# Performance work log

Measured on AMD Instinct MI355X. Metric: run time of the kernel, lower is better.

## Reference

```python
import jax, jax.numpy as jnp
import numpy as np

B, S, HID, NH, DH = 2, 1024, 4096, 32, 128
ACT_BITS, W_BITS = 8, 4
NEG_INF = float(np.finfo(np.float32).min)


def _qdq(x, bits):
    """Symmetric fake-quant over the last axis (per-token / per-out-channel), with STE."""
    qmax = 2.0 ** (bits - 1) - 1
    s = jnp.maximum(jnp.max(jnp.abs(x), axis=-1, keepdims=True) / qmax, 1e-8)
    q = jnp.clip(jnp.round(x / s), -qmax - 1, qmax) * s
    return x + jax.lax.stop_gradient(q - x)


def _rope_tables(seq_len, dim):
    inv_freq = 1.0 / (10000.0 ** (np.arange(0, dim, 2, dtype=np.float32) / dim))
    t = np.arange(seq_len, dtype=np.float32)
    freqs = np.outer(t, inv_freq)              # [S, DH/2]
    emb = np.concatenate([freqs, freqs], -1)   # [S, DH]
    return jnp.asarray(np.cos(emb)), jnp.asarray(np.sin(emb))


def _rotate_half(x):
    h = x.shape[-1] // 2
    return jnp.concatenate([-x[..., h:], x[..., :h]], axis=-1)


def _norm(x):
    return jnp.linalg.norm(x, axis=-1, keepdims=True)


def setup_inputs() -> dict:
    key = jax.random.key(0)
    ks = jax.random.split(key, 5)
    causal = jnp.where(jnp.tril(jnp.ones((S, S), dtype=bool)), 0.0, NEG_INF).astype(jnp.float32)
    return {
        "hidden_states": jax.random.normal(ks[0], (B, S, HID), jnp.float32),
        "wq": jax.random.normal(ks[1], (HID, HID), jnp.float32) * 0.02,
        "wk": jax.random.normal(ks[2], (HID, HID), jnp.float32) * 0.02,
        "wv": jax.random.normal(ks[3], (HID, HID), jnp.float32) * 0.02,
        "wo": jax.random.normal(ks[4], (HID, HID), jnp.float32) * 0.02,
        "attention_mask": jnp.broadcast_to(causal[None, None], (B, 1, S, S)),
    }


def reference(hidden_states, wq, wk, wv, wo, attention_mask):
    cos, sin = _rope_tables(S, DH)
    cos, sin = cos[None, None], sin[None, None]          # [1,1,S,DH]
    x = _qdq(hidden_states, ACT_BITS)                    # act fake-quant (per token)

    def proj(w):
        return jnp.einsum('bsh,dh->bsd', x, _qdq(w, W_BITS)).reshape(B, S, NH, DH).transpose(0, 2, 1, 3)

    q, k, v = proj(wq), proj(wk), proj(wv)               # [B,H,S,D]
    q = q * cos + _rotate_half(q) * sin
    k = k * cos + _rotate_half(k) * sin

    # qkt_matmul: quant Q and K, rescale scores by quantization norm ratios a1, a2
    x1len = _norm(q)
    qq = _qdq(q, ACT_BITS)
    a1 = _norm(qq) / x1len                               # [B,H,S,1]
    x2len = _norm(k)
    kq = _qdq(k, ACT_BITS)
    a2 = jnp.swapaxes(_norm(kq) / x2len, 2, 3)           # [B,H,1,S]

    attn = jnp.einsum('bhqd,bhkd->bhqk', qq, kq) / np.float32(np.sqrt(DH))
    attn = attn / a1 / a2
    attn = attn + attention_mask
    attn = jnp.maximum(attn, NEG_INF)
    p = jax.nn.softmax(attn.astype(jnp.float32), axis=-1)

    # pv_matmul: quant P and V, rescale output by V's norm ratio
    pq = _qdq(p, ACT_BITS)
    x2len_v = _norm(v)
    vq = _qdq(v, ACT_BITS)
    a2v = _norm(vq) / x2len_v                            # [B,H,S,1]

    out = jnp.einsum('bhqk,bhkd->bhqd', pq, vq) / a2v    # [B,H,S,D]
    out = out.transpose(0, 2, 1, 3).reshape(B, S, HID)
    out = jnp.einsum('bsh,dh->bsd', _qdq(out, ACT_BITS), _qdq(wo, W_BITS))
    return out
```

## Files before the change

kernel.cpp:

```cpp
#include <hip/hip_runtime.h>
#include <hip/hip_bf16.h>
#include <math.h>
#include <stdint.h>

#define NEG_INF_F (-3.4028234663852886e38f)

typedef __bf16 bf16_t;
typedef __bf16 bf16x8 __attribute__((ext_vector_type(8)));
typedef float f32x4 __attribute__((ext_vector_type(4)));
typedef float f32x16 __attribute__((ext_vector_type(16)));
typedef int i32x4 __attribute__((ext_vector_type(4)));
typedef int i32x16 __attribute__((ext_vector_type(16)));
typedef int8_t c8x4 __attribute__((ext_vector_type(4)));

static constexpr int Bb = 2, Ss = 1024, Hid = 4096, Nh = 32, Dh = 128;
static constexpr int Mr = Bb * Ss;
static constexpr int Bh = Bb * Nh;

__device__ __forceinline__ void gload_lds16(const void* g, void* l) {
  __builtin_amdgcn_global_load_lds((const __attribute__((address_space(1))) void*)g,
                                   (__attribute__((address_space(3))) void*)l, 16, 0, 0);
}

__device__ __forceinline__ float wred_max(float v) {
#pragma unroll
  for (int off = 32; off > 0; off >>= 1) v = fmaxf(v, __shfl_xor(v, off));
  return v;
}

__device__ __forceinline__ unsigned pkbf(float a, float b) {
  unsigned short ua = __builtin_bit_cast(unsigned short, (bf16_t)a);
  unsigned short ub = __builtin_bit_cast(unsigned short, (bf16_t)b);
  return (unsigned)ua | ((unsigned)ub << 16);
}

__global__ void rope_table_kernel(float* __restrict__ ctab, float* __restrict__ stab) {
  int i = blockIdx.x * 256 + threadIdx.x;
  int srow = i >> 6, d = i & 63;
  float invf = (float)pow(10000.0, -((double)(2 * d) / (double)Dh));
  float ang = (float)srow * invf;
  ctab[i] = (float)cos((double)ang);
  stab[i] = (float)sin((double)ang);
}

__device__ __forceinline__ void quant_row_body(
    const float* __restrict__ x, int8_t* __restrict__ o, float* __restrict__ scale,
    int row, int ncols, float qmax, float clo, float chi)
{
  const int tid = threadIdx.x;
  const float4* x4 = (const float4*)x;
  const int n4 = ncols >> 2;
  float m = 0.f;
  for (int i = tid; i < n4; i += 256) {
    float4 v = x4[i];
    m = fmaxf(m, fmaxf(fmaxf(fabsf(v.x), fabsf(v.y)), fmaxf(fabsf(v.z), fabsf(v.w))));
  }
  m = wred_max(m);
  __shared__ float red[4];
  if ((tid & 63) == 0) red[tid >> 6] = m;
  __syncthreads();
  m = fmaxf(fmaxf(red[0], red[1]), fmaxf(red[2], red[3]));
  const float s = fmaxf(m / qmax, 1e-8f);
  if (tid == 0) scale[row] = s;
  c8x4* o4 = (c8x4*)o;
  for (int i = tid; i < n4; i += 256) {
    float4 v = x4[i];
    c8x4 r;
    r[0] = (int8_t)(int)fminf(fmaxf(rintf(v.x / s), clo), chi);
    r[1] = (int8_t)(int)fminf(fmaxf(rintf(v.y / s), clo), chi);
    r[2] = (int8_t)(int)fminf(fmaxf(rintf(v.z / s), clo), chi);
    r[3] = (int8_t)(int)fminf(fmaxf(rintf(v.w / s), clo), chi);
    o4[i] = r;
  }
}

__global__ __launch_bounds__(256) void quant_rows_kernel(
    const float* __restrict__ in, int8_t* __restrict__ outq,
    float* __restrict__ scale, int ncols, float qmax, float clo, float chi)
{
  const int row = blockIdx.x;
  quant_row_body(in + (size_t)row * ncols, outq + (size_t)row * ncols, scale,
                 row, ncols, qmax, clo, chi);
}

__global__ __launch_bounds__(256) void quant_w3_kernel(
    const float* __restrict__ w0, const float* __restrict__ w1, const float* __restrict__ w2,
    int8_t* __restrict__ o0, int8_t* __restrict__ o1, int8_t* __restrict__ o2,
    float* __restrict__ s0, float* __restrict__ s1, float* __restrict__ s2)
{
  const int sel = blockIdx.x >> 12, row = blockIdx.x & 4095;
  const float* in = sel == 0 ? w0 : (sel == 1 ? w1 : w2);
  int8_t* o = sel == 0 ? o0 : (sel == 1 ? o1 : o2);
  float* sc = sel == 0 ? s0 : (sel == 1 ? s1 : s2);
  quant_row_body(in + (size_t)row * Hid, o + (size_t)row * Hid, sc, row, Hid,
                 7.f, -8.f, 7.f);
}

#define GEMM_PHASE(Abuf, Bbuf)                                                        \
  {                                                                                   \
    i32x4 af[4], bw[4];                                                               \
    _Pragma("unroll")                                                                 \
    for (int f = 0; f < 4; ++f) {                                                     \
      af[f] = *(const i32x4*)&(Abuf)[(wm * 64 + f * 16 + l15) * 64 + ck];             \
      bw[f] = *(const i32x4*)&(Bbuf)[(f * 32 + wn * 16 + l15) * 64 + ck];             \
    }                                                                                 \
    _Pragma("unroll")                                                                 \
    for (int fm = 0; fm < 4; ++fm)                                                    \
      _Pragma("unroll")                                                               \
      for (int fn = 0; fn < 4; ++fn)                                                  \
        acc[fm][fn] = __builtin_amdgcn_mfma_i32_16x16x64_i8(af[fm], bw[fn],           \
                                                            acc[fm][fn], 0, 0, 0);   \
  }

#define GEMM_STAGE(koff, Abuf, Bbuf)                                                  \
  gload_lds16(gA + (koff), (Abuf) + wid * 1024);                                      \
  gload_lds16(gA + (koff) + rstep, (Abuf) + 4096 + wid * 1024);                       \
  gload_lds16(gB + (koff), (Bbuf) + wid * 1024);                                      \
  gload_lds16(gB + (koff) + rstep, (Bbuf) + 4096 + wid * 1024);

#define GEMM_CORE_DBUF(SMEM)                                                          \
  int8_t* A0 = (int8_t*)(SMEM);                                                       \
  int8_t* A1 = (int8_t*)(SMEM) + 8192;                                                \
  int8_t* B0 = (int8_t*)(SMEM) + 16384;                                               \
  int8_t* B1 = (int8_t*)(SMEM) + 24576;                                               \
  const int srowL = tid >> 2;                                                         \
  const int schunk = ((tid & 3) ^ ((tid >> 3) & 3)) * 16;                             \
  const int8_t* gA = A + (size_t)(bm + srowL) * K + schunk;                           \
  const int8_t* gB = W + (size_t)(bn + srowL) * K + schunk;                           \
  const size_t rstep = (size_t)64 * K;                                                \
  const int ck = (kg4 ^ ((l15 >> 1) & 3)) * 16;                                       \
  i32x4 acc[4][4] = {};                                                               \
  GEMM_STAGE(0, A0, B0)                                                               \
  __syncthreads();                                                                    \
  for (int k0 = 0; k0 < K; k0 += 128) {                                               \
    if (k0 + 64 < K) { GEMM_STAGE(k0 + 64, A1, B1) }                                  \
    GEMM_PHASE(A0, B0)                                                                \
    __syncthreads();                                                                  \
    if (k0 + 128 < K) { GEMM_STAGE(k0 + 128, A0, B0) }                                \
    GEMM_PHASE(A1, B1)                                                                \
    __syncthreads();                                                                  \
  }

__global__ __launch_bounds__(256) void qkv_gemm_kernel(
    const int8_t* __restrict__ A, const float* __restrict__ sA,
    const int8_t* __restrict__ wqz, const int8_t* __restrict__ wkz, const int8_t* __restrict__ wvz,
    const float* __restrict__ swq, const float* __restrict__ swk, const float* __restrict__ swv,
    int8_t* __restrict__ qqb, float* __restrict__ Fq,
    int8_t* __restrict__ kqb, float* __restrict__ Fk,
    bf16_t* __restrict__ vdq, float* __restrict__ a2vp,
    const float* __restrict__ ctab, const float* __restrict__ stab)
{
  __shared__ __align__(16) char smem[34816 + 3072];
  float (*s_red)[128][3] = (float (*)[128][3])(smem + 34816);

  const int tid = threadIdx.x, lane = tid & 63, wid = tid >> 6;
  const int id = blockIdx.x;
  const int xcd = id & 7, within = id >> 3;
  const int nIdx = xcd * 12 + (within >> 4);
  const int mIdx = within & 15;
  const int wsel = nIdx >> 5, head = nIdx & 31;
  const int bm = mIdx * 128, bn = head * 128;
  const int8_t* W = wsel == 0 ? wqz : (wsel == 1 ? wkz : wvz);
  const float* sW = wsel == 0 ? swq : (wsel == 1 ? swk : swv);
  constexpr int K = Hid;

  const int wm = wid >> 1, wn = wid & 1;
  const int l15 = lane & 15, kg4 = lane >> 4;

  GEMM_CORE_DBUF(smem)

  float sav[4][4], swv_[4];
#pragma unroll
  for (int fm = 0; fm < 4; ++fm)
#pragma unroll
    for (int j = 0; j < 4; ++j) sav[fm][j] = sA[bm + wm * 64 + fm * 16 + kg4 * 4 + j];
#pragma unroll
  for (int fn = 0; fn < 4; ++fn) swv_[fn] = sW[bn + fn * 32 + wn * 16 + l15];

  float val[4][4][4];
#pragma unroll
  for (int fm = 0; fm < 4; ++fm)
#pragma unroll
    for (int fn = 0; fn < 4; ++fn)
#pragma unroll
      for (int j = 0; j < 4; ++j)
        val[fm][fn][j] = (float)acc[fm][fn][j] * sav[fm][j] * swv_[fn];

  const int b = bm >> 10;
  const int bh = b * Nh + head;
  float r_[4][4][4];
  if (wsel != 2) {
    const int dmA = wn * 16 + l15, dmB = 32 + wn * 16 + l15;
#pragma unroll
    for (int fm = 0; fm < 4; ++fm)
#pragma unroll
      for (int j = 0; j < 4; ++j) {
        const int srow = (bm + wm * 64 + fm * 16 + kg4 * 4 + j) & (Ss - 1);
        const float cA = ctab[srow * 64 + dmA], cB = ctab[srow * 64 + dmB];
        const float sA_ = stab[srow * 64 + dmA], sB_ = stab[srow * 64 + dmB];
        r_[fm][0][j] = __fsub_rn(__fmul_rn(val[fm][0][j], cA), __fmul_rn(val[fm][2][j], sA_));
        r_[fm][1][j] = __fsub_rn(__fmul_rn(val[fm][1][j], cB), __fmul_rn(val[fm][3][j], sB_));
        r_[fm][2][j] = __fadd_rn(__fmul_rn(val[fm][2][j], cA), __fmul_rn(val[fm][0][j], sA_));
        r_[fm][3][j] = __fadd_rn(__fmul_rn(val[fm][3][j], cB), __fmul_rn(val[fm][1][j], sB_));
      }
  } else {
#pragma unroll
    for (int fm = 0; fm < 4; ++fm)
#pragma unroll
      for (int fn = 0; fn < 4; ++fn)
#pragma unroll
        for (int j = 0; j < 4; ++j) r_[fm][fn][j] = val[fm][fn][j];
  }
  float ma_[4][4], n2_[4][4];
#pragma unroll
  for (int fm = 0; fm < 4; ++fm)
#pragma unroll
    for (int j = 0; j < 4; ++j) {
      float ma = 0.f, n2 = 0.f;
#pragma unroll
      for (int fn = 0; fn < 4; ++fn) {
        const float x = r_[fm][fn][j];
        ma = fmaxf(ma, fabsf(x));
        n2 += x * x;
      }
#pragma unroll
      for (int off = 1; off < 16; off <<= 1) {
        ma = fmaxf(ma, __shfl_xor(ma, off));
        n2 += __shfl_xor(n2, off);
      }
      ma_[fm][j] = ma;
      n2_[fm][j] = n2;
    }
  if (l15 == 0) {
#pragma unroll
    for (int fm = 0; fm < 4; ++fm)
#pragma unroll
      for (int j = 0; j < 4; ++j) {
        const int rl = wm * 64 + fm * 16 + kg4 * 4 + j;
        s_red[wn][rl][0] = ma_[fm][j];
        s_red[wn][rl][1] = n2_[fm][j];
      }
  }
  __syncthreads();
  float qc[4][4][4], svl[4][4], n2c[4][4], nq2_[4][4];
#pragma unroll
  for (int fm = 0; fm < 4; ++fm)
#pragma unroll
    for (int j = 0; j < 4; ++j) {
      const int rl = wm * 64 + fm * 16 + kg4 * 4 + j;
      const float ma = fmaxf(ma_[fm][j], s_red[wn ^ 1][rl][0]);
      const float n2 = n2_[fm][j] + s_red[wn ^ 1][rl][1];
      const float s = fmaxf(ma / 127.0f, 1e-8f);
      float nq2 = 0.f;
#pragma unroll
      for (int fn = 0; fn < 4; ++fn) {
        const float q = fminf(fmaxf(rintf(r_[fm][fn][j] / s), -128.f), 127.f);
        qc[fm][fn][j] = q;
        nq2 += q * q;
      }
#pragma unroll
      for (int off = 1; off < 16; off <<= 1) nq2 += __shfl_xor(nq2, off);
      svl[fm][j] = s;
      n2c[fm][j] = n2;
      nq2_[fm][j] = nq2;
    }
  __syncthreads();
  if (l15 == 0) {
#pragma unroll
    for (int fm = 0; fm < 4; ++fm)
#pragma unroll
      for (int j = 0; j < 4; ++j)
        s_red[wn][wm * 64 + fm * 16 + kg4 * 4 + j][2] = nq2_[fm][j];
  }
  __syncthreads();

  if (wsel != 2) {
    int8_t* outq = (wsel == 0) ? qqb : kqb;
    float* Ff = (wsel == 0) ? Fq : Fk;
#pragma unroll
    for (int fm = 0; fm < 4; ++fm)
#pragma unroll
      for (int j = 0; j < 4; ++j) {
        const int rl = wm * 64 + fm * 16 + kg4 * 4 + j;
        const int stok = (bm + rl) & (Ss - 1);
        const size_t rowBase = ((size_t)bh * Ss + stok) * Dh;
#pragma unroll
        for (int fn = 0; fn < 4; ++fn)
          outq[rowBase + fn * 32 + wn * 16 + l15] = (int8_t)(int)qc[fm][fn][j];
        if (wn == 0 && l15 == 0) {
          const float nq2 = nq2_[fm][j] + s_red[1][rl][2];
          Ff[(size_t)bh * Ss + stok] = sqrtf(n2c[fm][j] / nq2) * 0.2973017787506803f;
        }
      }
  } else {
    bf16_t* svt = (bf16_t*)smem;
#pragma unroll
    for (int fm = 0; fm < 4; ++fm)
#pragma unroll
      for (int j = 0; j < 4; ++j) {
        const int t = wm * 64 + fm * 16 + kg4 * 4 + j;
#pragma unroll
        for (int fn = 0; fn < 4; ++fn) {
          const int d = fn * 32 + wn * 16 + l15;
          svt[d * 136 + t] = (bf16_t)(qc[fm][fn][j] * svl[fm][j]);
        }
        if (wn == 0 && l15 == 0) {
          const float nq2 = nq2_[fm][j] + s_red[1][t][2];
          a2vp[(size_t)bh * Ss + ((bm + t) & (Ss - 1))] =
              svl[fm][j] * sqrtf(nq2) / sqrtf(n2c[fm][j]);
        }
      }
    __syncthreads();
    const int d = tid >> 1, toff = (tid & 1) * 64;
    const int s0 = bm & (Ss - 1);
    const bf16_t* src = svt + d * 136 + toff;
    bf16_t* dst = vdq + ((size_t)bh * Dh + d) * Ss + s0 + toff;
#pragma unroll
    for (int k = 0; k < 8; ++k) {
      bf16x8 tv;
#pragma unroll
      for (int e = 0; e < 8; ++e) tv[e] = src[k * 8 + e];
      *(bf16x8*)(dst + k * 8) = tv;
    }
  }
}

__global__ __launch_bounds__(256) void gemm0_kernel(
    const int8_t* __restrict__ A, const float* __restrict__ sA,
    const int8_t* __restrict__ W, const float* __restrict__ sW,
    float* __restrict__ out, int M, int N, int K)
{
  __shared__ __align__(16) char smem[32768];
  const int tid = threadIdx.x, lane = tid & 63, wid = tid >> 6;
  const int id = blockIdx.x;
  const int xcd = id & 7, within = id >> 3;
  const int nIdx = xcd * 4 + (within >> 4);
  const int mIdx = within & 15;
  const int bm = mIdx * 128, bn = nIdx * 128;
  const int wm = wid >> 1, wn = wid & 1;
  const int l15 = lane & 15, kg4 = lane >> 4;

  GEMM_CORE_DBUF(smem)

#pragma unroll
  for (int fm = 0; fm < 4; ++fm) {
#pragma unroll
    for (int j = 0; j < 4; ++j) {
      const int row = bm + wm * 64 + fm * 16 + kg4 * 4 + j;
      const float sa = sA[row];
#pragma unroll
      for (int fn = 0; fn < 4; ++fn) {
        const int col = bn + fn * 32 + wn * 16 + l15;
        out[(size_t)row * N + col] = (float)acc[fm][fn][j] * sa * sW[col];
      }
    }
  }
}

#define KR(r) (((r) & 3) + 8 * ((r) >> 2) + 4 * hi)
__global__ __launch_bounds__(64, 2) void attn_kernel(
    const int8_t* __restrict__ qq, const int8_t* __restrict__ kq,
    const bf16_t* __restrict__ vdqt,
    const float* __restrict__ Fq, const float* __restrict__ Fk,
    const float* __restrict__ A2v, float* __restrict__ oattn)
{
  const int bh = blockIdx.x, b = bh >> 5, h = bh & 31;
  const int lane = threadIdx.x & 63;
  const int l31 = lane & 31, hi = lane >> 5;
  const int u = 31 - (int)blockIdx.y;
  const int q0 = u * 32;
  const int nt = u + 1;
  const size_t bhS = (size_t)bh * Ss;

  const int8_t* qrow = qq + (bhS + q0 + l31) * Dh + hi * 16;
  i32x4 qf[4];
#pragma unroll
  for (int c = 0; c < 4; ++c) qf[c] = *(const i32x4*)(qrow + c * 32);
  const float fq = Fq[bhS + q0 + l31];
  const int qcol = q0 + l31;

  float m = NEG_INF_F;
  int t = 0;
  for (; t + 1 < nt; t += 2) {
    const int kb0 = t * 32, kb1 = kb0 + 32;
    const int8_t* kr0 = kq + (bhS + kb0 + l31) * Dh + hi * 16;
    const int8_t* kr1 = kq + (bhS + kb1 + l31) * Dh + hi * 16;
    i32x16 ca = {}, cb = {}, da = {}, db = {};
    ca = __builtin_amdgcn_mfma_i32_32x32x32_i8(*(const i32x4*)(kr0),      qf[0], ca, 0, 0, 0);
    cb = __builtin_amdgcn_mfma_i32_32x32x32_i8(*(const i32x4*)(kr0 + 64), qf[2], cb, 0, 0, 0);
    da = __builtin_amdgcn_mfma_i32_32x32x32_i8(*(const i32x4*)(kr1),      qf[0], da, 0, 0, 0);
    db = __builtin_amdgcn_mfma_i32_32x32x32_i8(*(const i32x4*)(kr1 + 64), qf[2], db, 0, 0, 0);
    ca = __builtin_amdgcn_mfma_i32_32x32x32_i8(*(const i32x4*)(kr0 + 32), qf[1], ca, 0, 0, 0);
    cb = __builtin_amdgcn_mfma_i32_32x32x32_i8(*(const i32x4*)(kr0 + 96), qf[3], cb, 0, 0, 0);
    da = __builtin_amdgcn_mfma_i32_32x32x32_i8(*(const i32x4*)(kr1 + 32), qf[1], da, 0, 0, 0);
    db = __builtin_amdgcn_mfma_i32_32x32x32_i8(*(const i32x4*)(kr1 + 96), qf[3], db, 0, 0, 0);
    float4 fk40[4], fk41[4];
#pragma unroll
    for (int g = 0; g < 4; ++g) fk40[g] = *(const float4*)&Fk[bhS + kb0 + g * 8 + 4 * hi];
#pragma unroll
    for (int g = 0; g < 4; ++g) fk41[g] = *(const float4*)&Fk[bhS + kb1 + g * 8 + 4 * hi];
    const bool diag1 = (t + 1 == nt - 1);
#pragma unroll
    for (int r = 0; r < 16; ++r) {
      m = fmaxf(m, (float)(ca[r] + cb[r]) * fq * ((const float*)&fk40[r >> 2])[r & 3]);
      const float v1 = (float)(da[r] + db[r]) * fq * ((const float*)&fk41[r >> 2])[r & 3];
      if (!diag1 || (kb1 + KR(r) <= qcol)) m = fmaxf(m, v1);
    }
  }
  if (t < nt) {
    const int kb = t * 32;
    const int8_t* krow = kq + (bhS + kb + l31) * Dh + hi * 16;
    i32x16 ca = {}, cb = {};
    ca = __builtin_amdgcn_mfma_i32_32x32x32_i8(*(const i32x4*)(krow),      qf[0], ca, 0, 0, 0);
    cb = __builtin_amdgcn_mfma_i32_32x32x32_i8(*(const i32x4*)(krow + 64), qf[2], cb, 0, 0, 0);
    ca = __builtin_amdgcn_mfma_i32_32x32x32_i8(*(const i32x4*)(krow + 32), qf[1], ca, 0, 0, 0);
    cb = __builtin_amdgcn_mfma_i32_32x32x32_i8(*(const i32x4*)(krow + 96), qf[3], cb, 0, 0, 0);
    float4 fk4[4];
#pragma unroll
    for (int g = 0; g < 4; ++g) fk4[g] = *(const float4*)&Fk[bhS + kb + g * 8 + 4 * hi];
#pragma unroll
    for (int r = 0; r < 16; ++r) {
      const float v = (float)(ca[r] + cb[r]) * fq * ((const float*)&fk4[r >> 2])[r & 3];
      if (kb + KR(r) <= qcol) m = fmaxf(m, v);
    }
  }
  m = fmaxf(m, __shfl_xor(m, 32));

  float z = 0.f;
  f32x16 oacc[4] = {};
  for (int tt = 0; tt < nt; ++tt) {
    const int kb = tt * 32;
    const int8_t* krow = kq + (bhS + kb + l31) * Dh + hi * 16;
    i32x16 ca = {}, cb = {};
    ca = __builtin_amdgcn_mfma_i32_32x32x32_i8(*(const i32x4*)(krow),      qf[0], ca, 0, 0, 0);
    cb = __builtin_amdgcn_mfma_i32_32x32x32_i8(*(const i32x4*)(krow + 64), qf[2], cb, 0, 0, 0);
    ca = __builtin_amdgcn_mfma_i32_32x32x32_i8(*(const i32x4*)(krow + 32), qf[1], ca, 0, 0, 0);
    cb = __builtin_amdgcn_mfma_i32_32x32x32_i8(*(const i32x4*)(krow + 96), qf[3], cb, 0, 0, 0);
    float4 fk4[4];
#pragma unroll
    for (int g = 0; g < 4; ++g) fk4[g] = *(const float4*)&Fk[bhS + kb + g * 8 + 4 * hi];
    float p[16];
    const bool diag = (tt == nt - 1);
#pragma unroll
    for (int r = 0; r < 16; ++r) {
      float v = (float)(ca[r] + cb[r]) * fq * ((const float*)&fk4[r >> 2])[r & 3];
      if (diag && (kb + KR(r) > qcol)) v = NEG_INF_F;
      const float e = __expf(v - m);
      z += e;
      p[r] = rintf(127.0f * e);
    }
#pragma unroll
    for (int s = 0; s < 2; ++s) {
      const int rs = s * 8;
      unsigned k0 = pkbf(p[rs + 0], p[rs + 1]);
      unsigned k1 = pkbf(p[rs + 2], p[rs + 3]);
      unsigned k2 = pkbf(p[rs + 4], p[rs + 5]);
      unsigned k3 = pkbf(p[rs + 6], p[rs + 7]);
      unsigned sx0 = __shfl_xor(k0, 32);
      unsigned sx1 = __shfl_xor(k1, 32);
      unsigned sx2 = __shfl_xor(k2, 32);
      unsigned sx3 = __shfl_xor(k3, 32);
      uint4 ww;
      ww.x = hi ? sx2 : k0;
      ww.y = hi ? sx3 : k1;
      ww.z = hi ? k2 : sx0;
      ww.w = hi ? k3 : sx1;
      const bf16x8 af = __builtin_bit_cast(bf16x8, ww);
      const int kg2 = kb + s * 16 + hi * 8;
#pragma unroll
      for (int dt = 0; dt < 4; ++dt) {
        const bf16x8 vf = *(const bf16x8*)(vdqt + ((size_t)bh * Dh + dt * 32 + l31) * Ss + kg2);
        oacc[dt] = __builtin_amdgcn_mfma_f32_32x32x16_bf16(af, vf, oacc[dt], 0, 0, 0);
      }
    }
  }
  z += __shfl_xor(z, 32);
  const float osc = (1.0f / z) / 127.0f / A2v[bhS + q0 + l31];
#pragma unroll
  for (int dt = 0; dt < 4; ++dt) {
#pragma unroll
    for (int r = 0; r < 16; ++r) {
      const int q = q0 + KR(r);
      const float oscr = __shfl(osc, KR(r));
      oattn[((size_t)b * Ss + q) * Hid + h * Dh + dt * 32 + l31] = oacc[dt][r] * oscr;
    }
  }
}

extern "C" void kernel_launch(void* const* d_in, const int* in_sizes, int n_in,
                              void* d_out, int out_size, void* d_ws, size_t ws_size,
                              hipStream_t stream)
{
  const float* hidden = (const float*)d_in[0];
  const float* wq = (const float*)d_in[1];
  const float* wk = (const float*)d_in[2];
  const float* wv = (const float*)d_in[3];
  const float* wo = (const float*)d_in[4];
  float* out = (float*)d_out;

  char* p = (char*)d_ws;
  auto alloc = [&](size_t bytes) -> char* {
    char* r = p; p += (bytes + 255) & ~(size_t)255; return r;
  };
  int8_t* xq   = (int8_t*)alloc((size_t)Mr * Hid);
  int8_t* wb0  = (int8_t*)alloc((size_t)Hid * Hid);
  int8_t* wb1  = (int8_t*)alloc((size_t)Hid * Hid);
  int8_t* wb2  = (int8_t*)alloc((size_t)Hid * Hid);
  float*  oat  = (float*) alloc((size_t)Bh * Ss * Dh * sizeof(float));
  int8_t* qqb  = (int8_t*)alloc((size_t)Bh * Ss * Dh);
  int8_t* kqb  = (int8_t*)alloc((size_t)Bh * Ss * Dh);
  bf16_t* vdqt = (bf16_t*)alloc((size_t)Bh * Dh * Ss * sizeof(bf16_t));
  float* sxa = (float*)alloc((size_t)Mr * sizeof(float));
  float* sw0 = (float*)alloc((size_t)Hid * sizeof(float));
  float* sw1 = (float*)alloc((size_t)Hid * sizeof(float));
  float* sw2 = (float*)alloc((size_t)Hid * sizeof(float));
  float* Fq  = (float*)alloc((size_t)Bh * Ss * sizeof(float));
  float* Fk  = (float*)alloc((size_t)Bh * Ss * sizeof(float));
  float* A2v = (float*)alloc((size_t)Bh * Ss * sizeof(float));
  float* soa = (float*)alloc((size_t)Mr * sizeof(float));
  float* ctab = (float*)alloc((size_t)Ss * 64 * sizeof(float));
  float* stab = (float*)alloc((size_t)Ss * 64 * sizeof(float));
  int8_t* oq  = xq;

  rope_table_kernel<<<Ss * 64 / 256, 256, 0, stream>>>(ctab, stab);
  quant_rows_kernel<<<Mr, 256, 0, stream>>>(hidden, xq, sxa, Hid, 127.f, -128.f, 127.f);
  quant_w3_kernel<<<3 * Hid, 256, 0, stream>>>(wq, wk, wv, wb0, wb1, wb2, sw0, sw1, sw2);

  qkv_gemm_kernel<<<1536, 256, 0, stream>>>(xq, sxa, wb0, wb1, wb2, sw0, sw1, sw2,
                                            qqb, Fq, kqb, Fk, vdqt, A2v, ctab, stab);

  dim3 ga(Bh, 32);
  attn_kernel<<<ga, 64, 0, stream>>>(qqb, kqb, vdqt, Fq, Fk, A2v, oat);

  quant_rows_kernel<<<Mr, 256, 0, stream>>>(oat, oq, soa, Hid, 127.f, -128.f, 127.f);
  quant_rows_kernel<<<Hid, 256, 0, stream>>>(wo, wb0, sw0, Hid, 7.f, -8.f, 7.f);
  gemm0_kernel<<<512, 256, 0, stream>>>(oq, soa, wb0, sw0, out, Mr, Hid, Hid);
}
```

Measured before the change: 391.4 us.

## Deepen int8 GEMM pipeline with 128-wide K stages and explicit vmcnt barriers

Reworks the shared int8 GEMM core used by the QKV and output projections. Each LDS stage now holds a 128-deep K slice instead of 64, with a new XOR swizzle over 8 chunks. Loads are issued two stages ahead, and explicit s_waitcnt vmcnt plus raw s_barrier replace __syncthreads, so global-to-LDS copies overlap MFMA work and barriers per K step drop. LDS use roughly doubles to 64KB+ per block, which may reduce occupancy.

```diff
diff --git a/kernel.cpp b/kernel.cpp
--- a/kernel.cpp
+++ b/kernel.cpp
@@ -96,13 +96,33 @@
                  7.f, -8.f, 7.f);
 }
 
-#define GEMM_PHASE(Abuf, Bbuf)                                                        \
-  {                                                                                   \
+#define GEMM_WAITBAR(N)                                                               \
+  asm volatile("s_waitcnt vmcnt(" #N ")" ::: "memory");                               \
+  __builtin_amdgcn_sched_barrier(0);                                                  \
+  __builtin_amdgcn_s_barrier();                                                       \
+  __builtin_amdgcn_sched_barrier(0);
+
+#define GEMM_BARONLY                                                                  \
+  __builtin_amdgcn_sched_barrier(0);                                                  \
+  __builtin_amdgcn_s_barrier();                                                       \
+  __builtin_amdgcn_sched_barrier(0);
+
+#define GEMM_STAGE128(koff, Abuf, Bbuf)                                               \
+  _Pragma("unroll")                                                                   \
+  for (int r = 0; r < 4; ++r) {                                                       \
+    gload_lds16(gA + (koff) + (size_t)r * 32 * K, (Abuf) + r * 4096 + wid * 1024);    \
+    gload_lds16(gB + (koff) + (size_t)r * 32 * K, (Bbuf) + r * 4096 + wid * 1024);    \
+  }
+
+#define GEMM_PHASE128(Abuf, Bbuf)                                                     \
+  _Pragma("unroll")                                                                   \
+  for (int g = 0; g < 2; ++g) {                                                       \
     i32x4 af[4], bw[4];                                                               \
     _Pragma("unroll")                                                                 \
     for (int f = 0; f < 4; ++f) {                                                     \
-      af[f] = *(const i32x4*)&(Abuf)[(wm * 64 + f * 16 + l15) * 64 + ck];             \
-      bw[f] = *(const i32x4*)&(Bbuf)[(f * 32 + wn * 16 + l15) * 64 + ck];             \
+      const int ca = (((g << 2) | kg4) ^ (l15 & 7)) * 16;                             \
+      af[f] = *(const i32x4*)&(Abuf)[(wm * 64 + f * 16 + l15) * 128 + ca];            \
+      bw[f] = *(const i32x4*)&(Bbuf)[(f * 32 + wn * 16 + l15) * 128 + ca];            \
     }                                                                                 \
     _Pragma("unroll")                                                                 \
     for (int fm = 0; fm < 4; ++fm)                                                    \
@@ -112,34 +132,33 @@
                                                             acc[fm][fn], 0, 0, 0);   \
   }
 
-#define GEMM_STAGE(koff, Abuf, Bbuf)                                                  \
-  gload_lds16(gA + (koff), (Abuf) + wid * 1024);                                      \
-  gload_lds16(gA + (koff) + rstep, (Abuf) + 4096 + wid * 1024);                       \
-  gload_lds16(gB + (koff), (Bbuf) + wid * 1024);                                      \
-  gload_lds16(gB + (koff) + rstep, (Bbuf) + 4096 + wid * 1024);
-
-#define GEMM_CORE_DBUF(SMEM)                                                          \
+#define GEMM_CORE_PIPE(SMEM)                                                          \
   int8_t* A0 = (int8_t*)(SMEM);                                                       \
-  int8_t* A1 = (int8_t*)(SMEM) + 8192;                                                \
-  int8_t* B0 = (int8_t*)(SMEM) + 16384;                                               \
-  int8_t* B1 = (int8_t*)(SMEM) + 24576;                                               \
-  const int srowL = tid >> 2;                                                         \
-  const int schunk = ((tid & 3) ^ ((tid >> 3) & 3)) * 16;                             \
-  const int8_t* gA = A + (size_t)(bm + srowL) * K + schunk;                           \
-  const int8_t* gB = W + (size_t)(bn + srowL) * K + schunk;                           \
-  const size_t rstep = (size_t)64 * K;                                                \
-  const int ck = (kg4 ^ ((l15 >> 1) & 3)) * 16;                                       \
+  int8_t* A1 = (int8_t*)(SMEM) + 16384;                                               \
+  int8_t* B0 = (int8_t*)(SMEM) + 32768;                                               \
+  int8_t* B1 = (int8_t*)(SMEM) + 49152;                                               \
+  const int strow = wid * 8 + (lane >> 3);                                            \
+  const int schunk = ((lane & 7) ^ (lane >> 3)) * 16;                                 \
+  const int8_t* gA = A + (size_t)(bm + strow) * K + schunk;                           \
+  const int8_t* gB = W + (size_t)(bn + strow) * K + schunk;                           \
   i32x4 acc[4][4] = {};                                                               \
-  GEMM_STAGE(0, A0, B0)                                                               \
-  __syncthreads();                                                                    \
-  for (int k0 = 0; k0 < K; k0 += 128) {                                               \
-    if (k0 + 64 < K) { GEMM_STAGE(k0 + 64, A1, B1) }                                  \
-    GEMM_PHASE(A0, B0)                                                                \
-    __syncthreads();                                                                  \
-    if (k0 + 128 < K) { GEMM_STAGE(k0 + 128, A0, B0) }                                \
-    GEMM_PHASE(A1, B1)                                                                \
-    __syncthreads();                                                                  \
-  }
+  GEMM_STAGE128(0, A0, B0)                                                            \
+  GEMM_STAGE128(128, A1, B1)                                                          \
+  for (int k0 = 0; k0 + 512 <= K; k0 += 256) {                                        \
+    GEMM_WAITBAR(8)                                                                   \
+    GEMM_PHASE128(A0, B0)                                                             \
+    GEMM_BARONLY                                                                      \
+    GEMM_STAGE128(k0 + 256, A0, B0)                                                   \
+    GEMM_WAITBAR(8)                                                                   \
+    GEMM_PHASE128(A1, B1)                                                             \
+    GEMM_BARONLY                                                                      \
+    GEMM_STAGE128(k0 + 384, A1, B1)                                                   \
+  }                                                                                   \
+  GEMM_WAITBAR(8)                                                                     \
+  GEMM_PHASE128(A0, B0)                                                               \
+  GEMM_BARONLY                                                                        \
+  GEMM_WAITBAR(0)                                                                     \
+  GEMM_PHASE128(A1, B1)
 
 __global__ __launch_bounds__(256) void qkv_gemm_kernel(
     const int8_t* __restrict__ A, const float* __restrict__ sA,
@@ -150,8 +169,8 @@
     bf16_t* __restrict__ vdq, float* __restrict__ a2vp,
     const float* __restrict__ ctab, const float* __restrict__ stab)
 {
-  __shared__ __align__(16) char smem[34816 + 3072];
-  float (*s_red)[128][3] = (float (*)[128][3])(smem + 34816);
+  __shared__ __align__(16) char smem[65536 + 3072];
+  float (*s_red)[128][3] = (float (*)[128][3])(smem + 65536);
 
   const int tid = threadIdx.x, lane = tid & 63, wid = tid >> 6;
   const int id = blockIdx.x;
@@ -167,7 +186,7 @@
   const int wm = wid >> 1, wn = wid & 1;
   const int l15 = lane & 15, kg4 = lane >> 4;
 
-  GEMM_CORE_DBUF(smem)
+  GEMM_CORE_PIPE(smem)
 
   float sav[4][4], swv_[4];
 #pragma unroll
@@ -330,7 +349,7 @@
     const int8_t* __restrict__ W, const float* __restrict__ sW,
     float* __restrict__ out, int M, int N, int K)
 {
-  __shared__ __align__(16) char smem[32768];
+  __shared__ __align__(16) char smem[65536];
   const int tid = threadIdx.x, lane = tid & 63, wid = tid >> 6;
   const int id = blockIdx.x;
   const int xcd = id & 7, within = id >> 3;
@@ -340,7 +359,7 @@
   const int wm = wid >> 1, wn = wid & 1;
   const int l15 = lane & 15, kg4 = lane >> 4;
 
-  GEMM_CORE_DBUF(smem)
+  GEMM_CORE_PIPE(smem)
 
 #pragma unroll
   for (int fm = 0; fm < 4; ++fm) {
```

Result: faster. 373.3 us (-4.6%).
